# Optimization experiments

Hardware: AMD Instinct MI355X
Metric: run time of the kernel (lower is better)

Reference implementation:

```python
import jax, jax.numpy as jnp
import numpy as np

N = 100000; E = 1600000; G = 2000; S = 40; MAXP = 50
IN = 64; F = 128; H = 4; HD = F // H; FFN = 8 * F
EPS = 1e-5; BN_EPS = 1e-5

def _ln(x, g, b):
    m = jnp.mean(x, -1, keepdims=True)
    v = jnp.mean((x - m) ** 2, -1, keepdims=True)
    return (x - m) * jax.lax.rsqrt(v + EPS) * g + b

def setup_inputs():
    key = jax.random.key(0)
    ks = jax.random.split(key, 16)
    def lin(k, i, o):
        kw, kb = jax.random.split(k)
        lim = 1.0 / np.sqrt(i)
        return (jax.random.uniform(kw, (i, o), jnp.float32, -lim, lim),
                jax.random.uniform(kb, (o,), jnp.float32, -lim, lim))
    W_gcn, b_gcn = lin(ks[1], IN, F)
    Wq, bq = lin(ks[2], F, F); Wk, bk = lin(ks[3], F, F)
    Wv, bv = lin(ks[4], F, F); Wo, bo = lin(ks[5], F, F)
    W1, b1 = lin(ks[6], F, FFN); W2, b2 = lin(ks[7], FFN, F)
    Wg, bg = lin(ks[8], 2 * F, F)
    ones = lambda: jnp.ones((F,), jnp.float32)
    zeros = lambda: jnp.zeros((F,), jnp.float32)
    return {
        'x': jax.random.normal(ks[0], (N, IN), jnp.float32),
        'edge_index': jax.random.randint(ks[9], (2, E), 0, N),
        'batch': jnp.repeat(jnp.arange(G), N // G),
        'set_batch': jnp.repeat(jnp.arange(S), G // S),
        'W_gcn': W_gcn, 'b_gcn': b_gcn,
        'bn_g': ones(), 'bn_b': zeros(),
        'lnpre_g': ones(), 'lnpre_b': zeros(),
        'Wq': Wq, 'bq': bq, 'Wk': Wk, 'bk': bk, 'Wv': Wv, 'bv': bv, 'Wo': Wo, 'bo': bo,
        'ln1_g': ones(), 'ln1_b': zeros(),
        'W1': W1, 'b1': b1, 'W2': W2, 'b2': b2,
        'ln2_g': ones(), 'ln2_b': zeros(),
        'Wg': Wg, 'bg': bg,
    }

def _forward(x, W_gcn, b_gcn, bn_g, bn_b, lnpre_g, lnpre_b, Wq, bq, Wk, bk, Wv, bv, Wo, bo, ln1_g, ln1_b, W1, b1, W2, b2, ln2_g, ln2_b, Wg, bg, edge_index, batch, set_batch):
    row, col = edge_index[0], edge_index[1]
    # GCNConv, improved=True -> self-loop weight 2.0 (PyG gcn_norm)
    xw = x @ W_gcn                                              # [N,F]
    deg = jax.ops.segment_sum(jnp.ones(E, xw.dtype), col, N) + 2.0
    dinv = jax.lax.rsqrt(deg)
    norm = dinv[row] * dinv[col]                                # [E]
    agg = jax.ops.segment_sum(xw[row] * norm[:, None], col, N)  # scatter-add to targets
    h = agg + (2.0 * dinv * dinv)[:, None] * xw + b_gcn
    # BatchNorm1d eval (running_mean=0, running_var=1) + ReLU; dropout is identity in eval
    h = jax.nn.relu(h * jax.lax.rsqrt(jnp.asarray(1.0 + BN_EPS, h.dtype)) * bn_g + bn_b)
    # global mean pool per graph
    cnt_g = jax.ops.segment_sum(jnp.ones(N, h.dtype), batch, G)
    z = jax.ops.segment_sum(h, batch, G) / cnt_g[:, None]       # [G,F]
    # to_dense_batch over sets (set_batch is sorted)
    cnt_s = jax.ops.segment_sum(jnp.ones(G, jnp.int32), set_batch, S)
    starts = jnp.cumsum(cnt_s) - cnt_s
    pos = jnp.arange(G) - starts[set_batch]                     # position within set
    zd = jnp.zeros((S, MAXP, F), z.dtype).at[set_batch, pos].set(z)
    mask = jnp.arange(MAXP)[None, :] < cnt_s[:, None]           # [S,MAXP]
    # pre-LN MHA with key_padding_mask
    zn = _ln(zd, lnpre_g, lnpre_b)
    q = (zn @ Wq + bq).reshape(S, MAXP, H, HD)
    k = (zn @ Wk + bk).reshape(S, MAXP, H, HD)
    v = (zn @ Wv + bv).reshape(S, MAXP, H, HD)
    scores = jnp.einsum('sqhd,skhd->shqk', q, k) / np.sqrt(HD)
    scores = jnp.where(mask[:, None, None, :], scores, -1e9)
    attn = jax.nn.softmax(scores, -1)
    o = jnp.einsum('shqk,skhd->sqhd', attn, v).reshape(S, MAXP, F) @ Wo + bo
    zd = _ln(zd + o, ln1_g, ln1_b)
    # FFN block (post-LN residual)
    f = jax.nn.relu(zd @ W1 + b1) @ W2 + b2
    zd = _ln(zd + f, ln2_g, ln2_b)
    # z_dense[mask] ordering == gather via (set_batch, pos); broadcast to nodes
    set_info = zd[set_batch, pos][batch]                        # [N,F]
    # gated fusion
    gate = jax.nn.sigmoid(jnp.concatenate([h, set_info], -1) @ Wg + bg)
    return gate * set_info + (1.0 - gate) * h

def reference(x, edge_index, batch, set_batch, W_gcn, b_gcn, bn_g, bn_b, lnpre_g, lnpre_b, Wq, bq, Wk, bk, Wv, bv, Wo, bo, ln1_g, ln1_b, W1, b1, W2, b2, ln2_g, ln2_b, Wg, bg):
    return _forward(x, W_gcn, b_gcn, bn_g, bn_b, lnpre_g, lnpre_b, Wq, bq, Wk, bk, Wv, bv, Wo, bo, ln1_g, ln1_b, W1, b1, W2, b2, ln2_g, ln2_b, Wg, bg, edge_index, batch, set_batch)
```

## Files before the change

### kernel.cpp

```cpp
#include <hip/hip_runtime.h>
#include <hip/hip_bf16.h>
#include <cstddef>

#define NN 100000
#define NE 1600000
#define NG 2000
#define NS 40
#define INF 64
#define F 128
#define FFN_DIM 1024
#define NB 782
#define BCAP 3072
#define SC_BLOCKS 512
#define SC_CHUNK 3125
#define KSPLIT 8

using bf16 = __hip_bfloat16;
typedef __attribute__((ext_vector_type(8))) short short8;
typedef __attribute__((ext_vector_type(4))) float f32x4;
typedef __attribute__((ext_vector_type(2))) float f32x2;

__device__ __forceinline__ short f2bs(float f){
    union { bf16 b; short s; } u; u.b = __float2bfloat16(f); return u.s;
}
__device__ __forceinline__ unsigned int pk2(float a, float b){
    return (unsigned int)(unsigned short)f2bs(a) | ((unsigned int)(unsigned short)f2bs(b) << 16);
}

__global__ __launch_bounds__(1024) void k_binit(int* __restrict__ bcursor){
    int t = threadIdx.x;
    if (t < NB) bcursor[t] = t * BCAP;
}

__global__ __launch_bounds__(256) void k_wcvt(const float* __restrict__ Wg, unsigned short* __restrict__ Wgb){
    int t = blockIdx.x*256 + threadIdx.x;
    for (int i=t; i<16384; i+=16*256){
        int k = i >> 7, n = i & 127;
        Wgb[n*128 + k] = (unsigned short)f2bs(Wg[(size_t)k*F + n]);
    }
}

__global__ __launch_bounds__(256) void k_xws(const float* __restrict__ x, const float* __restrict__ W,
                                             const float* __restrict__ dinv, unsigned char* __restrict__ xws8){
    __shared__ short Xs[128*72];
    __shared__ short Ws[128*72];
    int t = threadIdx.x;
    int rowBase = blockIdx.x * 128;
    #pragma unroll
    for (int i=0;i<32;i++){
        int id = i*256+t; int k = id>>7, n = id&127;
        Ws[n*72 + k] = f2bs(W[id]);
    }
    #pragma unroll
    for (int i=0;i<8;i++){
        int id = i*256+t;
        int r = id>>4; int k4 = (id&15)*4;
        int row = rowBase + r; if (row >= NN) row = NN-1;
        float4 v = *(const float4*)&x[(size_t)row*INF + k4];
        *(unsigned int*)&Xs[r*72 + k4]     = pk2(v.x, v.y);
        *(unsigned int*)&Xs[r*72 + k4 + 2] = pk2(v.z, v.w);
    }
    __syncthreads();
    int lane = t & 63, w = t >> 6;
    int lr = lane & 15, quad = lane >> 4;
    f32x4 acc[2][8];
    #pragma unroll
    for (int i=0;i<2;i++)
        #pragma unroll
        for (int j=0;j<8;j++) acc[i][j] = (f32x4){0.f,0.f,0.f,0.f};
    #pragma unroll
    for (int ks=0; ks<2; ++ks){
        int kb = ks*32 + quad*8;
        short8 b0 = *(const short8*)&Xs[((w  )*16 + lr)*72 + kb];
        short8 b1 = *(const short8*)&Xs[((w+4)*16 + lr)*72 + kb];
        #pragma unroll
        for (int mt=0; mt<8; ++mt){
            short8 a = *(const short8*)&Ws[(mt*16 + lr)*72 + kb];
            acc[0][mt] = __builtin_amdgcn_mfma_f32_16x16x32_bf16(a, b0, acc[0][mt], 0, 0, 0);
            acc[1][mt] = __builtin_amdgcn_mfma_f32_16x16x32_bf16(a, b1, acc[1][mt], 0, 0, 0);
        }
    }
    #pragma unroll
    for (int rt=0; rt<2; ++rt){
        int row = rowBase + (w + rt*4)*16 + lr;
        if (row < NN){
            float dv = dinv[row];
            #pragma unroll
            for (int mt=0; mt<8; ++mt){
                int p = __builtin_amdgcn_cvt_pk_fp8_f32(acc[rt][mt][0]*dv, acc[rt][mt][1]*dv, 0, false);
                p     = __builtin_amdgcn_cvt_pk_fp8_f32(acc[rt][mt][2]*dv, acc[rt][mt][3]*dv, p, true);
                *(int*)&xws8[(size_t)row*F + mt*16 + quad*4] = p;
            }
        }
    }
}

__global__ __launch_bounds__(1024) void k_scatter2(const int* __restrict__ ei, int* __restrict__ bcursor,
                                                   int* __restrict__ ebuf){
    __shared__ int lh[NB];
    __shared__ int lb[NB];
    int t = threadIdx.x;
    int base = blockIdx.x * SC_CHUNK;
    for (int b=t; b<NB; b+=1024) lh[b] = 0;
    __syncthreads();
    int rr[4], cc[4];
    #pragma unroll
    for (int q=0;q<4;q++){
        int i = t + q*1024;
        bool v = (i < SC_CHUNK);
        int idx = v ? (base + i) : base;
        rr[q] = ei[idx];
        cc[q] = ei[NE + idx];
        if (v) atomicAdd(&lh[cc[q]>>7], 1);
    }
    __syncthreads();
    for (int b=t; b<NB; b+=1024){
        int n = lh[b];
        lb[b] = n ? atomicAdd(&bcursor[b], n) : 0;
        lh[b] = 0;
    }
    __syncthreads();
    #pragma unroll
    for (int q=0;q<4;q++){
        int i = t + q*1024;
        if (i < SC_CHUNK){
            int b = cc[q] >> 7;
            int rk = atomicAdd(&lh[b], 1);
            ebuf[lb[b] + rk] = (rr[q] << 7) | (cc[q] & 127);
        }
    }
}

__global__ __launch_bounds__(256) void k_sort(const int* __restrict__ ebuf, const int* __restrict__ bcursor,
                                              int* __restrict__ cnt, float* __restrict__ dinv,
                                              int* __restrict__ nstart, int* __restrict__ ebuf2){
    __shared__ int lh[128];
    __shared__ int s[128];
    __shared__ int lcur[128];
    int t = threadIdx.x;
    int b = blockIdx.x;
    int e0 = b * BCAP;
    int nE = bcursor[b] - e0;
    if (t < 128) lh[t] = 0;
    __syncthreads();
    for (int i=t; i<nE; i+=256) atomicAdd(&lh[ebuf[e0+i] & 127], 1);
    __syncthreads();
    int c = (t < 128) ? lh[t] : 0;
    if (t < 128) s[t] = c;
    __syncthreads();
    #pragma unroll
    for (int off=1; off<128; off<<=1){
        int v = (t >= off && t < 128) ? s[t-off] : 0;
        __syncthreads();
        if (t < 128) s[t] += v;
        __syncthreads();
    }
    int node = b*128 + t;
    if (t < 128){
        int excl = s[t] - c;
        lcur[t] = excl;
        if (node < NN){
            nstart[node] = e0 + excl;
            cnt[node] = c;
            dinv[node] = rsqrtf((float)c + 2.0f);
        }
    }
    __syncthreads();
    for (int i=t; i<nE; i+=256){
        int v = ebuf[e0 + i];
        int nl = v & 127;
        int rk = atomicAdd(&lcur[nl], 1);
        ebuf2[e0 + rk] = (v >> 7) << 5;
    }
}

__global__ __launch_bounds__(256) void k_aggpool(const unsigned char* __restrict__ xws8,
                                                 const int* __restrict__ nstart, const int* __restrict__ cnt,
                                                 const float* __restrict__ dinv, const float* __restrict__ b_gcn,
                                                 const float* __restrict__ bn_g, const float* __restrict__ bn_b,
                                                 const int* __restrict__ ebuf2,
                                                 const float* __restrict__ lnpre_g, const float* __restrict__ lnpre_b,
                                                 float* __restrict__ h, unsigned short* __restrict__ hb,
                                                 float* __restrict__ z, float* __restrict__ zn,
                                                 unsigned short* __restrict__ znb){
    __shared__ float zacc[4][128];
    int t = threadIdx.x;
    int lane = t & 63, w = t >> 6;
    int half = lane >> 5, lh = lane & 31;
    int g = blockIdx.x;
    const unsigned int* xw32 = (const unsigned int*)xws8;
    unsigned int* hb32 = (unsigned int*)hb;
    unsigned int* znb32 = (unsigned int*)znb;

    float4 bg4  = *(const float4*)&b_gcn[4*lh];
    float4 bng4 = *(const float4*)&bn_g[4*lh];
    float4 bnb4 = *(const float4*)&bn_b[4*lh];
    const float bns = rsqrtf(1.f + 1e-5f);

    float za0=0.f, za1=0.f, za2=0.f, za3=0.f;

    for (int i = w; i < 50; i += 4){
        int node = g*50 + i;
        int s0n = nstart[node]; int dg = cnt[node]; float dv = dinv[node];
        unsigned int us = xw32[node*32 + lh];
        float a0=0.f, a1=0.f, a2=0.f, a3=0.f;
        int j=0;
        for (; j+8<=dg; j+=8){
            int r0 = ebuf2[s0n+j+0+half];
            int r1 = ebuf2[s0n+j+2+half];
            int r2 = ebuf2[s0n+j+4+half];
            int r3 = ebuf2[s0n+j+6+half];
            unsigned int u0 = xw32[r0 + lh];
            unsigned int u1 = xw32[r1 + lh];
            unsigned int u2 = xw32[r2 + lh];
            unsigned int u3 = xw32[r3 + lh];
            f32x2 l0 = __builtin_amdgcn_cvt_pk_f32_fp8(u0, false);
            f32x2 h0 = __builtin_amdgcn_cvt_pk_f32_fp8(u0, true);
            f32x2 l1 = __builtin_amdgcn_cvt_pk_f32_fp8(u1, false);
            f32x2 h1 = __builtin_amdgcn_cvt_pk_f32_fp8(u1, true);
            f32x2 l2 = __builtin_amdgcn_cvt_pk_f32_fp8(u2, false);
            f32x2 h2 = __builtin_amdgcn_cvt_pk_f32_fp8(u2, true);
            f32x2 l3 = __builtin_amdgcn_cvt_pk_f32_fp8(u3, false);
            f32x2 h3 = __builtin_amdgcn_cvt_pk_f32_fp8(u3, true);
            a0 += (l0.x + l1.x) + (l2.x + l3.x);
            a1 += (l0.y + l1.y) + (l2.y + l3.y);
            a2 += (h0.x + h1.x) + (h2.x + h3.x);
            a3 += (h0.y + h1.y) + (h2.y + h3.y);
        }
        for (; j+2<=dg; j+=2){
            int r0 = ebuf2[s0n+j+half];
            unsigned int u0 = xw32[r0 + lh];
            f32x2 l0 = __builtin_amdgcn_cvt_pk_f32_fp8(u0, false);
            f32x2 h0 = __builtin_amdgcn_cvt_pk_f32_fp8(u0, true);
            a0 += l0.x; a1 += l0.y; a2 += h0.x; a3 += h0.y;
        }
        if (j < dg && half == 0){
            int r0 = ebuf2[s0n+j];
            unsigned int u0 = xw32[r0 + lh];
            f32x2 l0 = __builtin_amdgcn_cvt_pk_f32_fp8(u0, false);
            f32x2 h0 = __builtin_amdgcn_cvt_pk_f32_fp8(u0, true);
            a0 += l0.x; a1 += l0.y; a2 += h0.x; a3 += h0.y;
        }
        a0 += __shfl_xor(a0, 32);
        a1 += __shfl_xor(a1, 32);
        a2 += __shfl_xor(a2, 32);
        a3 += __shfl_xor(a3, 32);
        f32x2 fl = __builtin_amdgcn_cvt_pk_f32_fp8(us, false);
        f32x2 fh = __builtin_amdgcn_cvt_pk_f32_fp8(us, true);
        float p0 = dv*(a0 + 2.f*fl.x) + bg4.x;
        float p1 = dv*(a1 + 2.f*fl.y) + bg4.y;
        float p2 = dv*(a2 + 2.f*fh.x) + bg4.z;
        float p3 = dv*(a3 + 2.f*fh.y) + bg4.w;
        p0 = fmaxf(p0*bns*bng4.x + bnb4.x, 0.f);
        p1 = fmaxf(p1*bns*bng4.y + bnb4.y, 0.f);
        p2 = fmaxf(p2*bns*bng4.z + bnb4.z, 0.f);
        p3 = fmaxf(p3*bns*bng4.w + bnb4.w, 0.f);
        if (half == 0){
            *(float4*)&h[(size_t)node*F + 4*lh] = make_float4(p0,p1,p2,p3);
            *(uint2*)&hb32[(size_t)node*64 + 2*lh] = make_uint2(pk2(p0,p1), pk2(p2,p3));
        }
        za0 += p0; za1 += p1; za2 += p2; za3 += p3;
    }
    if (half == 0)
        *(float4*)&zacc[w][4*lh] = make_float4(za0, za1, za2, za3);
    __syncthreads();
    if (w == 0){
        float4 v0 = *(const float4*)&zacc[0][4*lh];
        float4 v1 = *(const float4*)&zacc[1][4*lh];
        float4 v2 = *(const float4*)&zacc[2][4*lh];
        float4 v3 = *(const float4*)&zacc[3][4*lh];
        float s0 = ((v0.x+v1.x)+(v2.x+v3.x)) / 50.0f;
        float s1 = ((v0.y+v1.y)+(v2.y+v3.y)) / 50.0f;
        float s2 = ((v0.z+v1.z)+(v2.z+v3.z)) / 50.0f;
        float s3 = ((v0.w+v1.w)+(v2.w+v3.w)) / 50.0f;
        if (half == 0)
            *(float4*)&z[(size_t)g*F + 4*lh] = make_float4(s0,s1,s2,s3);
        float s = (s0+s1)+(s2+s3);
        #pragma unroll
        for (int off=1; off<32; off<<=1) s += __shfl_xor(s, off);
        float m = s * (1.f/128.f);
        float d0=s0-m, d1=s1-m, d2=s2-m, d3=s3-m;
        float vv = (d0*d0+d1*d1)+(d2*d2+d3*d3);
        #pragma unroll
        for (int off=1; off<32; off<<=1) vv += __shfl_xor(vv, off);
        float rs = rsqrtf(vv*(1.f/128.f) + 1e-5f);
        float4 lg = *(const float4*)&lnpre_g[4*lh];
        float4 lb = *(const float4*)&lnpre_b[4*lh];
        if (half == 0){
            float o0 = d0*rs*lg.x+lb.x, o1 = d1*rs*lg.y+lb.y;
            float o2 = d2*rs*lg.z+lb.z, o3 = d3*rs*lg.w+lb.w;
            *(float4*)&zn[(size_t)g*F + 4*lh] = make_float4(o0,o1,o2,o3);
            *(uint2*)&znb32[(size_t)g*64 + 2*lh] = make_uint2(pk2(o0,o1), pk2(o2,o3));
        }
    }
}

template<int RELU, int BF16OUT, int SPLITK>
__global__ __launch_bounds__(256) void k_mm_bf16(const unsigned short* __restrict__ A,
                                                 const float* __restrict__ B, const float* __restrict__ bias,
                                                 float* __restrict__ Cf, unsigned short* __restrict__ Cb,
                                                 int M, int K, int Nc){
    __shared__ short Bw[128*136];
    int t = threadIdx.x;
    int rowBase = blockIdx.x*128;
    int colBase = blockIdx.y*128;
    int kbeg = SPLITK ? blockIdx.z*128 : 0;
    #pragma unroll
    for (int i=0;i<64;i++){
        int id = i*256+t; int k = id>>7, n = id&127;
        Bw[n*136 + k] = f2bs(B[(size_t)(kbeg+k)*Nc + colBase + n]);
    }
    __syncthreads();
    int lane = t & 63, w = t >> 6;
    int lr = lane & 15, quad = lane >> 4;
    int mrow0 = rowBase + w*32;
    f32x4 acc[2][8];
    #pragma unroll
    for (int i=0;i<2;i++)
        #pragma unroll
        for (int j=0;j<8;j++) acc[i][j] = (f32x4){0.f,0.f,0.f,0.f};
    #pragma unroll
    for (int ks=0; ks<4; ++ks){
        int kb = ks*32 + quad*8;
        short8 a[2];
        #pragma unroll
        for (int mt=0; mt<2; ++mt){
            int row = mrow0 + mt*16 + lr;
            if (row >= M) row = M-1;
            a[mt] = *(const short8*)&A[(size_t)row*K + kbeg + kb];
        }
        #pragma unroll
        for (int nt=0; nt<8; ++nt){
            short8 b = *(const short8*)&Bw[(nt*16 + lr)*136 + kb];
            acc[0][nt] = __builtin_amdgcn_mfma_f32_16x16x32_bf16(a[0], b, acc[0][nt], 0, 0, 0);
            acc[1][nt] = __builtin_amdgcn_mfma_f32_16x16x32_bf16(a[1], b, acc[1][nt], 0, 0, 0);
        }
    }
    #pragma unroll
    for (int mt=0; mt<2; ++mt){
        #pragma unroll
        for (int r=0; r<4; ++r){
            int row = mrow0 + mt*16 + quad*4 + r;
            if (row >= M) continue;
            #pragma unroll
            for (int nt=0; nt<8; ++nt){
                int col = colBase + nt*16 + lr;
                float v = acc[mt][nt][r];
                if (!SPLITK){
                    v += bias[col];
                    if (RELU) v = fmaxf(v, 0.f);
                    if (BF16OUT) Cb[(size_t)row*Nc + col] = (unsigned short)f2bs(v);
                    else         Cf[(size_t)row*Nc + col] = v;
                } else {
                    Cf[(size_t)blockIdx.z*M*Nc + (size_t)row*Nc + col] = v;
                }
            }
        }
    }
}

__global__ __launch_bounds__(256) void k_qkv_mfma(const unsigned short* __restrict__ A,
                                                  const float* __restrict__ Wq, const float* __restrict__ Wk,
                                                  const float* __restrict__ Wv, const float* __restrict__ bq,
                                                  const float* __restrict__ bk, const float* __restrict__ bv,
                                                  float* __restrict__ Cq, float* __restrict__ Ck,
                                                  float* __restrict__ Cv){
    __shared__ short Bw[128*136];
    int t = threadIdx.x;
    int zsel = blockIdx.z;
    const float* B = (zsel==0) ? Wq : (zsel==1) ? Wk : Wv;
    const float* bias = (zsel==0) ? bq : (zsel==1) ? bk : bv;
    float* C = (zsel==0) ? Cq : (zsel==1) ? Ck : Cv;
    int rowBase = blockIdx.x*128;
    #pragma unroll
    for (int i=0;i<64;i++){
        int id = i*256+t; int k = id>>7, n = id&127;
        Bw[n*136 + k] = f2bs(B[(size_t)k*F + n]);
    }
    __syncthreads();
    int lane = t & 63, w = t >> 6;
    int lr = lane & 15, quad = lane >> 4;
    int mrow0 = rowBase + w*32;
    f32x4 acc[2][8];
    #pragma unroll
    for (int i=0;i<2;i++)
        #pragma unroll
        for (int j=0;j<8;j++) acc[i][j] = (f32x4){0.f,0.f,0.f,0.f};
    #pragma unroll
    for (int ks=0; ks<4; ++ks){
        int kb = ks*32 + quad*8;
        short8 a[2];
        #pragma unroll
        for (int mt=0; mt<2; ++mt){
            int row = mrow0 + mt*16 + lr;
            if (row >= NG) row = NG-1;
            a[mt] = *(const short8*)&A[(size_t)row*F + kb];
        }
        #pragma unroll
        for (int nt=0; nt<8; ++nt){
            short8 b = *(const short8*)&Bw[(nt*16 + lr)*136 + kb];
            acc[0][nt] = __builtin_amdgcn_mfma_f32_16x16x32_bf16(a[0], b, acc[0][nt], 0, 0, 0);
            acc[1][nt] = __builtin_amdgcn_mfma_f32_16x16x32_bf16(a[1], b, acc[1][nt], 0, 0, 0);
        }
    }
    #pragma unroll
    for (int mt=0; mt<2; ++mt){
        #pragma unroll
        for (int r=0; r<4; ++r){
            int row = mrow0 + mt*16 + quad*4 + r;
            if (row >= NG) continue;
            #pragma unroll
            for (int nt=0; nt<8; ++nt){
                int col = nt*16 + lr;
                C[(size_t)row*F + col] = acc[mt][nt][r] + bias[col];
            }
        }
    }
}

__global__ __launch_bounds__(256) void k_wo_ln(const float* __restrict__ ao, const float* __restrict__ Wo,
                                               const float* __restrict__ bo, const float* __restrict__ z,
                                               const float* __restrict__ g, const float* __restrict__ b,
                                               float* __restrict__ zd1, unsigned short* __restrict__ zd1b){
    __shared__ float As[32*36];
    __shared__ float Bs[32*128];
    int t = threadIdx.x;
    int rowBase = blockIdx.x*32;
    int c0 = (t&31)*4, r0 = (t>>5)*4;
    unsigned int* zd1b32 = (unsigned int*)zd1b;
    float acc[4][4];
    #pragma unroll
    for (int i=0;i<4;i++){ acc[i][0]=0.f; acc[i][1]=0.f; acc[i][2]=0.f; acc[i][3]=0.f; }
    for (int kb=0; kb<F; kb+=32){
        #pragma unroll
        for (int i=0;i<4;i++){
            int id = i*256+t; int kk = id&31; int r = id>>5;
            int row = rowBase + r;
            As[kk*36+r] = (row<NG) ? ao[(size_t)row*F + kb + kk] : 0.f;
        }
        #pragma unroll
        for (int i=0;i<16;i++){
            int id = i*256+t; int c = id&127; int kk = id>>7;
            Bs[kk*128+c] = Wo[(size_t)(kb+kk)*F + c];
        }
        __syncthreads();
        for (int kk=0;kk<32;kk++){
            float4 a = *(const float4*)&As[kk*36+r0];
            float4 bv = *(const float4*)&Bs[kk*128+c0];
            float av[4]={a.x,a.y,a.z,a.w}; float bb[4]={bv.x,bv.y,bv.z,bv.w};
            #pragma unroll
            for(int i=0;i<4;i++)
                #pragma unroll
                for(int j=0;j<4;j++) acc[i][j] += av[i]*bb[j];
        }
        __syncthreads();
    }
    float4 bo4 = *(const float4*)&bo[c0];
    float4 g4  = *(const float4*)&g[c0];
    float4 b4  = *(const float4*)&b[c0];
    #pragma unroll
    for (int i=0;i<4;i++){
        int row = rowBase + r0 + i;
        float v0=0.f,v1=0.f,v2=0.f,v3=0.f;
        if (row < NG){
            float4 zr = *(const float4*)&z[(size_t)row*F + c0];
            v0 = acc[i][0] + bo4.x + zr.x;
            v1 = acc[i][1] + bo4.y + zr.y;
            v2 = acc[i][2] + bo4.z + zr.z;
            v3 = acc[i][3] + bo4.w + zr.w;
        }
        float s = (v0+v1)+(v2+v3);
        #pragma unroll
        for (int off=1; off<32; off<<=1) s += __shfl_xor(s, off);
        float m = s * (1.f/128.f);
        float d0=v0-m, d1=v1-m, d2=v2-m, d3=v3-m;
        float vv = (d0*d0+d1*d1)+(d2*d2+d3*d3);
        #pragma unroll
        for (int off=1; off<32; off<<=1) vv += __shfl_xor(vv, off);
        float rs = rsqrtf(vv*(1.f/128.f) + 1e-5f);
        if (row < NG){
            float o0 = d0*rs*g4.x+b4.x, o1 = d1*rs*g4.y+b4.y;
            float o2 = d2*rs*g4.z+b4.z, o3 = d3*rs*g4.w+b4.w;
            *(float4*)&zd1[(size_t)row*F + c0] = make_float4(o0,o1,o2,o3);
            *(uint2*)&zd1b32[(size_t)row*(F/2) + c0/2] = make_uint2(pk2(o0,o1), pk2(o2,o3));
        }
    }
}

__global__ __launch_bounds__(256) void k_ln_red_gsi(const float* __restrict__ A, const float* __restrict__ part,
                                                    const float* __restrict__ bias, const float* __restrict__ g,
                                                    const float* __restrict__ b, const float* __restrict__ Wb,
                                                    const float* __restrict__ bg, float* __restrict__ zd2,
                                                    float* __restrict__ gsi){
    __shared__ float Zs[4][128];
    __shared__ float Bs[32*128];
    int t = threadIdx.x; int lane = t&63;
    int rquad = t>>6;
    int row = blockIdx.x*4 + rquad;
    int i0 = row*F + 2*lane;
    float x0 = A[i0] + bias[2*lane], x1 = A[i0+1] + bias[2*lane+1];
    #pragma unroll
    for (int zz=0; zz<KSPLIT; ++zz){
        x0 += part[(size_t)zz*NG*F + i0];
        x1 += part[(size_t)zz*NG*F + i0 + 1];
    }
    float s = x0+x1;
    for (int off=1; off<64; off<<=1) s += __shfl_xor(s, off);
    float m = s * (1.f/128.f);
    float d0 = x0-m, d1 = x1-m;
    float vv = d0*d0 + d1*d1;
    for (int off=1; off<64; off<<=1) vv += __shfl_xor(vv, off);
    float rs = rsqrtf(vv*(1.f/128.f) + 1e-5f);
    float o0 = d0*rs*g[2*lane]   + b[2*lane];
    float o1 = d1*rs*g[2*lane+1] + b[2*lane+1];
    zd2[i0]   = o0;
    zd2[i0+1] = o1;
    Zs[rquad][2*lane]   = o0;
    Zs[rquad][2*lane+1] = o1;
    __syncthreads();
    int col = t & 127, rp = t >> 7;
    float a0=0.f, a1=0.f;
    for (int kb=0; kb<F; kb+=32){
        #pragma unroll
        for (int i=0;i<16;i++){
            int id = i*256+t; int c = id&127; int kk = id>>7;
            Bs[kk*128+c] = Wb[(size_t)(kb+kk)*F + c];
        }
        __syncthreads();
        for (int kk=0;kk<32;kk++){
            float w = Bs[kk*128+col];
            a0 += Zs[rp][kb+kk]   * w;
            a1 += Zs[rp+2][kb+kk] * w;
        }
        __syncthreads();
    }
    float bgc = bg[col];
    gsi[(size_t)(blockIdx.x*4 + rp)*F + col]     = a0 + bgc;
    gsi[(size_t)(blockIdx.x*4 + rp + 2)*F + col] = a1 + bgc;
}

__global__ __launch_bounds__(256) void k_attn(const float* __restrict__ q, const float* __restrict__ k,
                                              const float* __restrict__ v, float* __restrict__ o){
    __shared__ float Qs[1600], Ks[1600], Vs[1600], Sc[2500];
    int t = threadIdx.x;
    int s = blockIdx.x >> 2; int hh = blockIdx.x & 3;
    for (int idx=t; idx<1600; idx+=256){
        int i = idx>>5, d = idx&31;
        size_t gi = (size_t)(s*50+i)*F + hh*32 + d;
        Qs[idx]=q[gi]; Ks[idx]=k[gi]; Vs[idx]=v[gi];
    }
    __syncthreads();
    for (int idx=t; idx<2500; idx+=256){
        int qi = idx/50, ki = idx%50;
        float acc=0.f;
        #pragma unroll 8
        for (int d=0;d<32;d++) acc += Qs[qi*32+d]*Ks[ki*32+d];
        Sc[idx] = acc * 0.17677669529663687f;
    }
    __syncthreads();
    if (t < 50){
        float m=-1e30f;
        for (int j=0;j<50;j++) m = fmaxf(m, Sc[t*50+j]);
        float sum=0.f;
        for (int j=0;j<50;j++){ float e=__expf(Sc[t*50+j]-m); Sc[t*50+j]=e; sum+=e; }
        float inv = 1.f/sum;
        for (int j=0;j<50;j++) Sc[t*50+j] *= inv;
    }
    __syncthreads();
    for (int idx=t; idx<1600; idx+=256){
        int qi = idx>>5, d = idx&31;
        float acc=0.f;
        #pragma unroll 10
        for (int ki=0;ki<50;ki++) acc += Sc[qi*50+ki]*Vs[ki*32+d];
        o[(size_t)(s*50+qi)*F + hh*32 + d] = acc;
    }
}

__global__ __launch_bounds__(256) void k_gate_mfma(const float* __restrict__ h,
                                                   const unsigned short* __restrict__ hb,
                                                   const unsigned short* __restrict__ Wgb,
                                                   const float* __restrict__ gsi, const float* __restrict__ zd2,
                                                   float* __restrict__ out){
    int t = threadIdx.x;
    int lane = t & 63, w = t >> 6;
    int lr = lane & 15, quad = lane >> 4;
    int mrow0 = blockIdx.x*64 + w*16;
    f32x4 acc[8];
    #pragma unroll
    for (int j=0;j<8;j++) acc[j] = (f32x4){0.f,0.f,0.f,0.f};
    #pragma unroll
    for (int ks=0; ks<4; ++ks){
        int kb = ks*32 + quad*8;
        int row = mrow0 + lr;
        if (row >= NN) row = NN-1;
        short8 a = *(const short8*)&hb[(size_t)row*F + kb];
        #pragma unroll
        for (int nt=0; nt<8; ++nt){
            short8 b = *(const short8*)&Wgb[(size_t)(nt*16 + lr)*128 + kb];
            acc[nt] = __builtin_amdgcn_mfma_f32_16x16x32_bf16(a, b, acc[nt], 0, 0, 0);
        }
    }
    #pragma unroll
    for (int r=0; r<4; ++r){
        int row = mrow0 + quad*4 + r;
        if (row >= NN) continue;
        int g = row / 50;
        const float* gs = &gsi[(size_t)g*F];
        const float* zs = &zd2[(size_t)g*F];
        const float* hr = &h[(size_t)row*F];
        float* orow = &out[(size_t)row*F];
        #pragma unroll
        for (int nt=0; nt<8; ++nt){
            int col = nt*16 + lr;
            float L = acc[nt][r] + gs[col];
            float gate = 1.f/(1.f + __expf(-L));
            orow[col] = gate*zs[col] + (1.f-gate)*hr[col];
        }
    }
}

extern "C" void kernel_launch(void* const* d_in, const int* in_sizes, int n_in,
                              void* d_out, int out_size, void* d_ws, size_t ws_size,
                              hipStream_t stream) {
    const float* x      = (const float*)d_in[0];
    const int*   ei     = (const int*)d_in[1];
    const float* W_gcn  = (const float*)d_in[4];
    const float* b_gcn  = (const float*)d_in[5];
    const float* bn_g   = (const float*)d_in[6];
    const float* bn_b   = (const float*)d_in[7];
    const float* lnpre_g= (const float*)d_in[8];
    const float* lnpre_b= (const float*)d_in[9];
    const float* Wq     = (const float*)d_in[10];
    const float* bq     = (const float*)d_in[11];
    const float* Wk     = (const float*)d_in[12];
    const float* bk     = (const float*)d_in[13];
    const float* Wv     = (const float*)d_in[14];
    const float* bv     = (const float*)d_in[15];
    const float* Wo     = (const float*)d_in[16];
    const float* bo     = (const float*)d_in[17];
    const float* ln1_g  = (const float*)d_in[18];
    const float* ln1_b  = (const float*)d_in[19];
    const float* W1     = (const float*)d_in[20];
    const float* b1     = (const float*)d_in[21];
    const float* W2     = (const float*)d_in[22];
    const float* b2     = (const float*)d_in[23];
    const float* ln2_g  = (const float*)d_in[24];
    const float* ln2_b  = (const float*)d_in[25];
    const float* Wg     = (const float*)d_in[26];
    const float* bg     = (const float*)d_in[27];
    float* out = (float*)d_out;
    char* ws = (char*)d_ws;

    size_t o = 0;
    unsigned char* xws8 = (unsigned char*)(ws + o); o += (size_t)NN*F;
    float* h     = (float*)(ws + o); o += (size_t)NN*F*4;
    unsigned short* hb = (unsigned short*)(ws + o); o += (size_t)NN*F*2;
    int*   cnt   = (int*)(ws + o);   o += (size_t)NN*4;
    int*   nstart= (int*)(ws + o);   o += (size_t)NN*4;
    int*   ebuf  = (int*)(ws + o);   o += (size_t)NB*BCAP*4;
    int*   ebuf2 = (int*)(ws + o);   o += (size_t)NB*BCAP*4;
    float* dinv  = (float*)(ws + o); o += (size_t)NN*4;
    int*   bcursor=(int*)(ws + o);   o += 1024*4;
    unsigned short* Wgb = (unsigned short*)(ws + o); o += 16384*2;
    float* z     = (float*)(ws + o); o += (size_t)NG*F*4;
    float* zn    = (float*)(ws + o); o += (size_t)NG*F*4;
    unsigned short* znb = (unsigned short*)(ws + o); o += (size_t)NG*F*2;
    float* qb    = (float*)(ws + o); o += (size_t)NG*F*4;
    float* kb2   = (float*)(ws + o); o += (size_t)NG*F*4;
    float* vb    = (float*)(ws + o); o += (size_t)NG*F*4;
    float* ao    = (float*)(ws + o); o += (size_t)NG*F*4;
    float* zd1   = (float*)(ws + o); o += (size_t)NG*F*4;
    unsigned short* zd1b = (unsigned short*)(ws + o); o += (size_t)NG*F*2;
    unsigned short* ffn1b = (unsigned short*)(ws + o); o += (size_t)NG*FFN_DIM*2;
    float* part  = (float*)(ws + o); o += (size_t)KSPLIT*NG*F*4;
    float* zd2   = (float*)(ws + o); o += (size_t)NG*F*4;
    float* gsi   = (float*)(ws + o); o += (size_t)NG*F*4;

    k_binit<<<1, 1024, 0, stream>>>(bcursor);
    k_wcvt<<<16, 256, 0, stream>>>(Wg, Wgb);
    k_scatter2<<<SC_BLOCKS, 1024, 0, stream>>>(ei, bcursor, ebuf);
    k_sort<<<NB, 256, 0, stream>>>(ebuf, bcursor, cnt, dinv, nstart, ebuf2);
    k_xws<<<(NN+127)/128, 256, 0, stream>>>(x, W_gcn, dinv, xws8);
    k_aggpool<<<NG, 256, 0, stream>>>(xws8, nstart, cnt, dinv, b_gcn, bn_g, bn_b, ebuf2,
                                      lnpre_g, lnpre_b, h, hb, z, zn, znb);

    dim3 gqkv((NG+127)/128, 1, 3);
    k_qkv_mfma<<<gqkv, 256, 0, stream>>>(znb, Wq, Wk, Wv, bq, bk, bv, qb, kb2, vb);
    k_attn<<<NS*4, 256, 0, stream>>>(qb, kb2, vb, ao);
    k_wo_ln<<<(NG+31)/32, 256, 0, stream>>>(ao, Wo, bo, z, ln1_g, ln1_b, zd1, zd1b);
    dim3 gffn1((NG+127)/128, FFN_DIM/128, 1);
    k_mm_bf16<1,1,0><<<gffn1, 256, 0, stream>>>(zd1b, W1, b1, nullptr, ffn1b, NG, F, FFN_DIM);
    dim3 gffn2((NG+127)/128, 1, KSPLIT);
    k_mm_bf16<0,0,1><<<gffn2, 256, 0, stream>>>(ffn1b, W2, nullptr, part, nullptr, NG, FFN_DIM, F);
    k_ln_red_gsi<<<NG/4, 256, 0, stream>>>(zd1, part, b2, ln2_g, ln2_b,
                                           Wg + (size_t)F*F, bg, zd2, gsi);

    k_gate_mfma<<<(NN+63)/64, 256, 0, stream>>>(h, hb, Wgb, gsi, zd2, out);
}
```

Measured before the change: 351.9 us.

## Pre-convert weights to bf16 once and read MFMA operands directly from global

Merges the bcursor init and the Wg conversion into a single init kernel. That kernel also converts Wq/Wk/Wv/W1/W2 to transposed bf16 copies, so the QKV and FFN MFMA kernels no longer convert fp32 weights into shared memory in every block. The GEMM kernels now use 64-row tiles that read B fragments straight from global/L2, which doubles the block count for better occupancy but gives up LDS reuse. It also stages the sorted edge list in shared memory so ebuf2 is written coalesced, and drops the unused fp32 zn output. The init kernel adds a serial transpose of about 1 MB of weights, with uncoalesced stores.

```diff
diff --git a/kernel.cpp b/kernel.cpp
--- a/kernel.cpp
+++ b/kernel.cpp
@@ -27,16 +27,30 @@
     return (unsigned int)(unsigned short)f2bs(a) | ((unsigned int)(unsigned short)f2bs(b) << 16);
 }
 
-__global__ __launch_bounds__(1024) void k_binit(int* __restrict__ bcursor){
-    int t = threadIdx.x;
-    if (t < NB) bcursor[t] = t * BCAP;
-}
-
-__global__ __launch_bounds__(256) void k_wcvt(const float* __restrict__ Wg, unsigned short* __restrict__ Wgb){
+__global__ __launch_bounds__(256) void k_initw(int* __restrict__ bcursor,
+                                               const float* __restrict__ Wq, const float* __restrict__ Wk,
+                                               const float* __restrict__ Wv, const float* __restrict__ W1,
+                                               const float* __restrict__ W2, const float* __restrict__ Wg,
+                                               unsigned short* __restrict__ Wqb, unsigned short* __restrict__ Wkb,
+                                               unsigned short* __restrict__ Wvb, unsigned short* __restrict__ W1b,
+                                               unsigned short* __restrict__ W2b, unsigned short* __restrict__ Wgb){
     int t = blockIdx.x*256 + threadIdx.x;
-    for (int i=t; i<16384; i+=16*256){
-        int k = i >> 7, n = i & 127;
-        Wgb[n*128 + k] = (unsigned short)f2bs(Wg[(size_t)k*F + n]);
+    int stride = gridDim.x*256;
+    for (int i=t; i<NB; i+=stride) bcursor[i] = i*BCAP;
+    for (int i=t; i<16384; i+=stride){
+        int k = i>>7, n = i&127;
+        Wqb[n*128+k] = (unsigned short)f2bs(Wq[(size_t)k*F+n]);
+        Wkb[n*128+k] = (unsigned short)f2bs(Wk[(size_t)k*F+n]);
+        Wvb[n*128+k] = (unsigned short)f2bs(Wv[(size_t)k*F+n]);
+        Wgb[n*128+k] = (unsigned short)f2bs(Wg[(size_t)k*F+n]);
+    }
+    for (int i=t; i<131072; i+=stride){
+        int k = i>>10, n = i&1023;
+        W1b[(size_t)n*128+k] = (unsigned short)f2bs(W1[(size_t)k*FFN_DIM+n]);
+    }
+    for (int i=t; i<131072; i+=stride){
+        int n = i>>10, k = i&1023;
+        W2b[(size_t)n*1024+k] = (unsigned short)f2bs(W2[(size_t)k*F+n]);
     }
 }
 
@@ -137,6 +151,7 @@
     __shared__ int lh[128];
     __shared__ int s[128];
     __shared__ int lcur[128];
+    __shared__ int sorted[BCAP];
     int t = threadIdx.x;
     int b = blockIdx.x;
     int e0 = b * BCAP;
@@ -170,8 +185,10 @@
         int v = ebuf[e0 + i];
         int nl = v & 127;
         int rk = atomicAdd(&lcur[nl], 1);
-        ebuf2[e0 + rk] = (v >> 7) << 5;
-    }
+        sorted[rk] = (v >> 7) << 5;
+    }
+    __syncthreads();
+    for (int i=t; i<nE; i+=256) ebuf2[e0 + i] = sorted[i];
 }
 
 __global__ __launch_bounds__(256) void k_aggpool(const unsigned char* __restrict__ xws8,
@@ -181,8 +198,7 @@
                                                  const int* __restrict__ ebuf2,
                                                  const float* __restrict__ lnpre_g, const float* __restrict__ lnpre_b,
                                                  float* __restrict__ h, unsigned short* __restrict__ hb,
-                                                 float* __restrict__ z, float* __restrict__ zn,
-                                                 unsigned short* __restrict__ znb){
+                                                 float* __restrict__ z, unsigned short* __restrict__ znb){
     __shared__ float zacc[4][128];
     int t = threadIdx.x;
     int lane = t & 63, w = t >> 6;
@@ -289,131 +305,122 @@
         if (half == 0){
             float o0 = d0*rs*lg.x+lb.x, o1 = d1*rs*lg.y+lb.y;
             float o2 = d2*rs*lg.z+lb.z, o3 = d3*rs*lg.w+lb.w;
-            *(float4*)&zn[(size_t)g*F + 4*lh] = make_float4(o0,o1,o2,o3);
             *(uint2*)&znb32[(size_t)g*64 + 2*lh] = make_uint2(pk2(o0,o1), pk2(o2,o3));
         }
     }
 }
 
-template<int RELU, int BF16OUT, int SPLITK>
-__global__ __launch_bounds__(256) void k_mm_bf16(const unsigned short* __restrict__ A,
-                                                 const float* __restrict__ B, const float* __restrict__ bias,
-                                                 float* __restrict__ Cf, unsigned short* __restrict__ Cb,
-                                                 int M, int K, int Nc){
-    __shared__ short Bw[128*136];
-    int t = threadIdx.x;
-    int rowBase = blockIdx.x*128;
-    int colBase = blockIdx.y*128;
-    int kbeg = SPLITK ? blockIdx.z*128 : 0;
-    #pragma unroll
-    for (int i=0;i<64;i++){
-        int id = i*256+t; int k = id>>7, n = id&127;
-        Bw[n*136 + k] = f2bs(B[(size_t)(kbeg+k)*Nc + colBase + n]);
-    }
-    __syncthreads();
+__global__ __launch_bounds__(256) void k_qkv_g(const unsigned short* __restrict__ znb,
+                                               const unsigned short* __restrict__ Wqb,
+                                               const unsigned short* __restrict__ Wkb,
+                                               const unsigned short* __restrict__ Wvb,
+                                               const float* __restrict__ bq, const float* __restrict__ bk,
+                                               const float* __restrict__ bv,
+                                               float* __restrict__ Cq, float* __restrict__ Ck,
+                                               float* __restrict__ Cv){
+    int zsel = blockIdx.z;
+    const unsigned short* B = (zsel==0)?Wqb:(zsel==1)?Wkb:Wvb;
+    const float* bias = (zsel==0)?bq:(zsel==1)?bk:bv;
+    float* C = (zsel==0)?Cq:(zsel==1)?Ck:Cv;
+    int t = threadIdx.x;
     int lane = t & 63, w = t >> 6;
     int lr = lane & 15, quad = lane >> 4;
-    int mrow0 = rowBase + w*32;
-    f32x4 acc[2][8];
-    #pragma unroll
-    for (int i=0;i<2;i++)
-        #pragma unroll
-        for (int j=0;j<8;j++) acc[i][j] = (f32x4){0.f,0.f,0.f,0.f};
+    int mrow0 = blockIdx.x*64 + w*16;
+    f32x4 acc[8];
+    #pragma unroll
+    for (int j=0;j<8;j++) acc[j] = (f32x4){0.f,0.f,0.f,0.f};
     #pragma unroll
     for (int ks=0; ks<4; ++ks){
         int kb = ks*32 + quad*8;
-        short8 a[2];
-        #pragma unroll
-        for (int mt=0; mt<2; ++mt){
-            int row = mrow0 + mt*16 + lr;
-            if (row >= M) row = M-1;
-            a[mt] = *(const short8*)&A[(size_t)row*K + kbeg + kb];
-        }
+        int row = mrow0 + lr;
+        if (row >= NG) row = NG-1;
+        short8 a = *(const short8*)&znb[(size_t)row*F + kb];
         #pragma unroll
         for (int nt=0; nt<8; ++nt){
-            short8 b = *(const short8*)&Bw[(nt*16 + lr)*136 + kb];
-            acc[0][nt] = __builtin_amdgcn_mfma_f32_16x16x32_bf16(a[0], b, acc[0][nt], 0, 0, 0);
-            acc[1][nt] = __builtin_amdgcn_mfma_f32_16x16x32_bf16(a[1], b, acc[1][nt], 0, 0, 0);
-        }
-    }
-    #pragma unroll
-    for (int mt=0; mt<2; ++mt){
-        #pragma unroll
-        for (int r=0; r<4; ++r){
-            int row = mrow0 + mt*16 + quad*4 + r;
-            if (row >= M) continue;
-            #pragma unroll
-            for (int nt=0; nt<8; ++nt){
-                int col = colBase + nt*16 + lr;
-                float v = acc[mt][nt][r];
-                if (!SPLITK){
-                    v += bias[col];
-                    if (RELU) v = fmaxf(v, 0.f);
-                    if (BF16OUT) Cb[(size_t)row*Nc + col] = (unsigned short)f2bs(v);
-                    else         Cf[(size_t)row*Nc + col] = v;
-                } else {
-                    Cf[(size_t)blockIdx.z*M*Nc + (size_t)row*Nc + col] = v;
-                }
-            }
-        }
-    }
-}
-
-__global__ __launch_bounds__(256) void k_qkv_mfma(const unsigned short* __restrict__ A,
-                                                  const float* __restrict__ Wq, const float* __restrict__ Wk,
-                                                  const float* __restrict__ Wv, const float* __restrict__ bq,
-                                                  const float* __restrict__ bk, const float* __restrict__ bv,
-                                                  float* __restrict__ Cq, float* __restrict__ Ck,
-                                                  float* __restrict__ Cv){
-    __shared__ short Bw[128*136];
-    int t = threadIdx.x;
-    int zsel = blockIdx.z;
-    const float* B = (zsel==0) ? Wq : (zsel==1) ? Wk : Wv;
-    const float* bias = (zsel==0) ? bq : (zsel==1) ? bk : bv;
-    float* C = (zsel==0) ? Cq : (zsel==1) ? Ck : Cv;
-    int rowBase = blockIdx.x*128;
-    #pragma unroll
-    for (int i=0;i<64;i++){
-        int id = i*256+t; int k = id>>7, n = id&127;
-        Bw[n*136 + k] = f2bs(B[(size_t)k*F + n]);
-    }
-    __syncthreads();
+            short8 b = *(const short8*)&B[(size_t)(nt*16 + lr)*128 + kb];
+            acc[nt] = __builtin_amdgcn_mfma_f32_16x16x32_bf16(a, b, acc[nt], 0, 0, 0);
+        }
+    }
+    #pragma unroll
+    for (int r=0; r<4; ++r){
+        int row = mrow0 + quad*4 + r;
+        if (row >= NG) continue;
+        #pragma unroll
+        for (int nt=0; nt<8; ++nt){
+            int col = nt*16 + lr;
+            C[(size_t)row*F + col] = acc[nt][r] + bias[col];
+        }
+    }
+}
+
+__global__ __launch_bounds__(256) void k_ffn1_g(const unsigned short* __restrict__ zd1b,
+                                                const unsigned short* __restrict__ W1b,
+                                                const float* __restrict__ b1,
+                                                unsigned short* __restrict__ ffn1b){
+    int t = threadIdx.x;
     int lane = t & 63, w = t >> 6;
     int lr = lane & 15, quad = lane >> 4;
-    int mrow0 = rowBase + w*32;
-    f32x4 acc[2][8];
-    #pragma unroll
-    for (int i=0;i<2;i++)
-        #pragma unroll
-        for (int j=0;j<8;j++) acc[i][j] = (f32x4){0.f,0.f,0.f,0.f};
+    int mrow0 = blockIdx.x*64 + w*16;
+    int colBase = blockIdx.y*128;
+    f32x4 acc[8];
+    #pragma unroll
+    for (int j=0;j<8;j++) acc[j] = (f32x4){0.f,0.f,0.f,0.f};
     #pragma unroll
     for (int ks=0; ks<4; ++ks){
         int kb = ks*32 + quad*8;
-        short8 a[2];
-        #pragma unroll
-        for (int mt=0; mt<2; ++mt){
-            int row = mrow0 + mt*16 + lr;
-            if (row >= NG) row = NG-1;
-            a[mt] = *(const short8*)&A[(size_t)row*F + kb];
-        }
+        int row = mrow0 + lr;
+        if (row >= NG) row = NG-1;
+        short8 a = *(const short8*)&zd1b[(size_t)row*F + kb];
         #pragma unroll
         for (int nt=0; nt<8; ++nt){
-            short8 b = *(const short8*)&Bw[(nt*16 + lr)*136 + kb];
-            acc[0][nt] = __builtin_amdgcn_mfma_f32_16x16x32_bf16(a[0], b, acc[0][nt], 0, 0, 0);
-            acc[1][nt] = __builtin_amdgcn_mfma_f32_16x16x32_bf16(a[1], b, acc[1][nt], 0, 0, 0);
-        }
-    }
-    #pragma unroll
-    for (int mt=0; mt<2; ++mt){
-        #pragma unroll
-        for (int r=0; r<4; ++r){
-            int row = mrow0 + mt*16 + quad*4 + r;
-            if (row >= NG) continue;
-            #pragma unroll
-            for (int nt=0; nt<8; ++nt){
-                int col = nt*16 + lr;
-                C[(size_t)row*F + col] = acc[mt][nt][r] + bias[col];
-            }
+            short8 b = *(const short8*)&W1b[(size_t)(colBase + nt*16 + lr)*128 + kb];
+            acc[nt] = __builtin_amdgcn_mfma_f32_16x16x32_bf16(a, b, acc[nt], 0, 0, 0);
+        }
+    }
+    #pragma unroll
+    for (int r=0; r<4; ++r){
+        int row = mrow0 + quad*4 + r;
+        if (row >= NG) continue;
+        #pragma unroll
+        for (int nt=0; nt<8; ++nt){
+            int col = colBase + nt*16 + lr;
+            ffn1b[(size_t)row*FFN_DIM + col] = (unsigned short)f2bs(fmaxf(acc[nt][r] + b1[col], 0.f));
+        }
+    }
+}
+
+__global__ __launch_bounds__(256) void k_ffn2_g(const unsigned short* __restrict__ ffn1b,
+                                                const unsigned short* __restrict__ W2b,
+                                                float* __restrict__ part){
+    int t = threadIdx.x;
+    int lane = t & 63, w = t >> 6;
+    int lr = lane & 15, quad = lane >> 4;
+    int mrow0 = blockIdx.x*64 + w*16;
+    int kbeg = blockIdx.z*128;
+    f32x4 acc[8];
+    #pragma unroll
+    for (int j=0;j<8;j++) acc[j] = (f32x4){0.f,0.f,0.f,0.f};
+    #pragma unroll
+    for (int ks=0; ks<4; ++ks){
+        int kb = ks*32 + quad*8;
+        int row = mrow0 + lr;
+        if (row >= NG) row = NG-1;
+        short8 a = *(const short8*)&ffn1b[(size_t)row*FFN_DIM + kbeg + kb];
+        #pragma unroll
+        for (int nt=0; nt<8; ++nt){
+            short8 b = *(const short8*)&W2b[(size_t)(nt*16 + lr)*1024 + kbeg + kb];
+            acc[nt] = __builtin_amdgcn_mfma_f32_16x16x32_bf16(a, b, acc[nt], 0, 0, 0);
+        }
+    }
+    float* Cp = part + (size_t)blockIdx.z*NG*F;
+    #pragma unroll
+    for (int r=0; r<4; ++r){
+        int row = mrow0 + quad*4 + r;
+        if (row >= NG) continue;
+        #pragma unroll
+        for (int nt=0; nt<8; ++nt){
+            int col = nt*16 + lr;
+            Cp[(size_t)row*F + col] = acc[nt][r];
         }
     }
 }
@@ -662,8 +669,12 @@
     float* dinv  = (float*)(ws + o); o += (size_t)NN*4;
     int*   bcursor=(int*)(ws + o);   o += 1024*4;
     unsigned short* Wgb = (unsigned short*)(ws + o); o += 16384*2;
+    unsigned short* Wqb = (unsigned short*)(ws + o); o += 16384*2;
+    unsigned short* Wkb = (unsigned short*)(ws + o); o += 16384*2;
+    unsigned short* Wvb = (unsigned short*)(ws + o); o += 16384*2;
+    unsigned short* W1b = (unsigned short*)(ws + o); o += (size_t)131072*2;
+    unsigned short* W2b = (unsigned short*)(ws + o); o += (size_t)131072*2;
     float* z     = (float*)(ws + o); o += (size_t)NG*F*4;
-    float* zn    = (float*)(ws + o); o += (size_t)NG*F*4;
     unsigned short* znb = (unsigned short*)(ws + o); o += (size_t)NG*F*2;
     float* qb    = (float*)(ws + o); o += (size_t)NG*F*4;
     float* kb2   = (float*)(ws + o); o += (size_t)NG*F*4;
@@ -676,22 +687,22 @@
     float* zd2   = (float*)(ws + o); o += (size_t)NG*F*4;
     float* gsi   = (float*)(ws + o); o += (size_t)NG*F*4;
 
-    k_binit<<<1, 1024, 0, stream>>>(bcursor);
-    k_wcvt<<<16, 256, 0, stream>>>(Wg, Wgb);
+    k_initw<<<64, 256, 0, stream>>>(bcursor, Wq, Wk, Wv, W1, W2, Wg,
+                                    Wqb, Wkb, Wvb, W1b, W2b, Wgb);
     k_scatter2<<<SC_BLOCKS, 1024, 0, stream>>>(ei, bcursor, ebuf);
     k_sort<<<NB, 256, 0, stream>>>(ebuf, bcursor, cnt, dinv, nstart, ebuf2);
     k_xws<<<(NN+127)/128, 256, 0, stream>>>(x, W_gcn, dinv, xws8);
     k_aggpool<<<NG, 256, 0, stream>>>(xws8, nstart, cnt, dinv, b_gcn, bn_g, bn_b, ebuf2,
-                                      lnpre_g, lnpre_b, h, hb, z, zn, znb);
-
-    dim3 gqkv((NG+127)/128, 1, 3);
-    k_qkv_mfma<<<gqkv, 256, 0, stream>>>(znb, Wq, Wk, Wv, bq, bk, bv, qb, kb2, vb);
+                                      lnpre_g, lnpre_b, h, hb, z, znb);
+
+    dim3 gqkv((NG+63)/64, 1, 3);
+    k_qkv_g<<<gqkv, 256, 0, stream>>>(znb, Wqb, Wkb, Wvb, bq, bk, bv, qb, kb2, vb);
     k_attn<<<NS*4, 256, 0, stream>>>(qb, kb2, vb, ao);
     k_wo_ln<<<(NG+31)/32, 256, 0, stream>>>(ao, Wo, bo, z, ln1_g, ln1_b, zd1, zd1b);
-    dim3 gffn1((NG+127)/128, FFN_DIM/128, 1);
-    k_mm_bf16<1,1,0><<<gffn1, 256, 0, stream>>>(zd1b, W1, b1, nullptr, ffn1b, NG, F, FFN_DIM);
-    dim3 gffn2((NG+127)/128, 1, KSPLIT);
-    k_mm_bf16<0,0,1><<<gffn2, 256, 0, stream>>>(ffn1b, W2, nullptr, part, nullptr, NG, FFN_DIM, F);
+    dim3 gffn1((NG+63)/64, FFN_DIM/128);
+    k_ffn1_g<<<gffn1, 256, 0, stream>>>(zd1b, W1b, b1, ffn1b);
+    dim3 gffn2((NG+63)/64, 1, KSPLIT);
+    k_ffn2_g<<<gffn2, 256, 0, stream>>>(ffn1b, W2b, part);
     k_ln_red_gsi<<<NG/4, 256, 0, stream>>>(zd1, part, b2, ln2_g, ln2_b,
                                            Wg + (size_t)F*F, bg, zd2, gsi);
 
```

Result: faster. 330.8 us (-6.0%).
